# Performance work log

Measured on AMD Instinct MI355X. Metric: run time of the kernel, lower is better.

## Reference

```python
import jax, jax.numpy as jnp
import numpy as np

DIM = 256
HID = 256
EPS = 1e-5

def _layernorm(x, g, b):
    mu = jnp.mean(x, axis=-1, keepdims=True)
    var = jnp.mean(jnp.square(x - mu), axis=-1, keepdims=True)
    return (x - mu) * jax.lax.rsqrt(var + EPS) * g + b

def setup_inputs() -> dict:
    key = jax.random.key(0)
    ks = jax.random.split(key, 6)
    B, N = 2, 512
    x = jax.random.normal(ks[0], (B, N, DIM), dtype=jnp.float32)
    mask = jax.random.randint(ks[1], (B, N), 0, 2).astype(jnp.bool_)
    s_in = 1.0 / np.sqrt(DIM)
    s_h = 1.0 / np.sqrt(HID)
    return {
        "x": x,
        "mask": mask,
        "ln_g": jnp.ones((DIM,), jnp.float32),
        "ln_b": jnp.zeros((DIM,), jnp.float32),
        "Wl": jax.random.uniform(ks[2], (DIM, HID), jnp.float32, -s_in, s_in),
        "bl": jnp.zeros((HID,), jnp.float32),
        "Wo": jax.random.uniform(ks[3], (HID, HID), jnp.float32, -s_h, s_h),
        "bo": jnp.zeros((HID,), jnp.float32),
        "lno_g": jnp.ones((HID,), jnp.float32),
        "lno_b": jnp.zeros((HID,), jnp.float32),
    }

def reference(x, mask, ln_g, ln_b, Wl, bl, Wo, bo, lno_g, lno_b):
    # x: [B, N, D], mask: [B, N] bool
    xn = _layernorm(x, ln_g, ln_b)
    left = xn @ Wl + bl                                  # [B, N, H]
    outer = left[:, :, None, :] * left[:, None, :, :]    # [B, N, N, H]
    m2 = (mask[:, :, None] & mask[:, None, :])[..., None]  # [B, N, N, 1]
    outer = jnp.where(m2, outer, 0.0)
    h = _layernorm(jax.nn.gelu(outer, approximate=False), lno_g, lno_b)
    return h @ Wo + bo                                   # [B, N, N, H]
```

## Files before the change

### kernel.cpp

```cpp
#include <hip/hip_runtime.h>
#include <stdint.h>

#define DIM 256
#define HID 256
#define NSEQ 512
#define NB 2
#define EPS 1e-5f

typedef __attribute__((ext_vector_type(4))) float f32x4;
typedef __attribute__((ext_vector_type(4))) short bf16x4;
typedef __attribute__((ext_vector_type(8))) short bf16x8;

#define DIAG_BLOCKS 512
#define BATCH_BLOCKS 2304

__device__ __forceinline__ unsigned short f2bf(float f) {
    unsigned int u = __float_as_uint(f);
    u += 0x7fffu + ((u >> 16) & 1u);
    return (unsigned short)(u >> 16);
}

__device__ __forceinline__ float bfval(float f) {
    return __uint_as_float((unsigned)f2bf(f) << 16);
}

__device__ __forceinline__ float gelu_fast(float x) {
    const float z  = x * 0.7071067811865476f;
    const float az = fabsf(z);
    const float t  = __builtin_amdgcn_rcpf(fmaf(0.3275911f, az, 1.0f));
    float p = fmaf(1.061405429f, t, -1.453152027f);
    p = fmaf(p, t,  1.421413741f);
    p = fmaf(p, t, -0.284496736f);
    p = fmaf(p, t,  0.254829592f);
    p = p * t;
    const float e = __builtin_amdgcn_exp2f(az * az * -1.4426950408889634f);
    float erfv = fmaf(-p, e, 1.0f);
    erfv = copysignf(erfv, z);
    return 0.5f * x * (1.0f + erfv);
}

__device__ __forceinline__ int pairpos(int k) {
    return ((k >> 5) << 5) + (((k >> 2) & 3) << 3) + (((k >> 4) & 1) << 2) + (k & 3);
}

__global__ __launch_bounds__(256) void prep_kernel(
    const float* __restrict__ x, const void* __restrict__ mask,
    const float* __restrict__ ln_g, const float* __restrict__ ln_b,
    const float* __restrict__ Wl, const float* __restrict__ bl,
    const float* __restrict__ Wo, const float* __restrict__ lno_b,
    const float* __restrict__ bo,
    float* __restrict__ lm, unsigned short* __restrict__ woTp,
    int* __restrict__ maskr, float* __restrict__ cst)
{
    const int row = blockIdx.x;
    const int t = threadIdx.x;
    const int lane = t & 63, w = t >> 6;
    __shared__ float xs[DIM];
    __shared__ float red[8];
    __shared__ int bad_s[4];

    {
        const int v = ((const int*)mask)[t];
        unsigned long long bm = __ballot((v & ~1) != 0);
        if (lane == 0) bad_s[w] = (bm != 0ull) ? 1 : 0;
    }

    float v = x[row * DIM + t];
    float s = v, ss = v * v;
    #pragma unroll
    for (int o = 32; o; o >>= 1) { s += __shfl_xor(s, o); ss += __shfl_xor(ss, o); }
    if (lane == 0) { red[w] = s; red[4 + w] = ss; }
    __syncthreads();
    s  = red[0] + red[1] + red[2] + red[3];
    ss = red[4] + red[5] + red[6] + red[7];
    const float mu  = s * (1.0f / DIM);
    const float var = ss * (1.0f / DIM) - mu * mu;
    const float rs  = rsqrtf(var + EPS);
    xs[t] = (v - mu) * rs * ln_g[t] + ln_b[t];
    __syncthreads();

    float acc = bl[t];
    #pragma unroll 4
    for (int k = 0; k < DIM; k += 4) {
        float4 xv = *(const float4*)&xs[k];
        acc = fmaf(xv.x, Wl[(k + 0) * HID + t], acc);
        acc = fmaf(xv.y, Wl[(k + 1) * HID + t], acc);
        acc = fmaf(xv.z, Wl[(k + 2) * HID + t], acc);
        acc = fmaf(xv.w, Wl[(k + 3) * HID + t], acc);
    }
    const int packed = bad_s[0] | bad_s[1] | bad_s[2] | bad_s[3];
    const int mv = packed ? (int)((const unsigned char*)mask)[row]
                          : ((const int*)mask)[row];
    lm[row * HID + t] = mv ? acc : 0.0f;
    if (t == 0) maskr[row] = mv;

    if (row < HID) {
        woTp[row * HID + pairpos(t)] = f2bf(Wo[t * HID + row]);
    }
    if (row == 0) {
        float c = bo[t];
        for (int k = 0; k < HID; ++k)
            c = fmaf(bfval(lno_b[k]), bfval(Wo[k * HID + t]), c);
        cst[t] = c;
    }
}

__global__ __launch_bounds__(256, 5) void outer_kernel(
    const float* __restrict__ lm, const unsigned short* __restrict__ woTp,
    const float* __restrict__ lno_g, const float* __restrict__ lno_b,
    const float* __restrict__ bo, const int* __restrict__ maskr,
    const float* __restrict__ cst, float* __restrict__ out)
{
    int blk = (int)blockIdx.x;
    int b = 0;
    if (blk >= BATCH_BLOCKS) { b = 1; blk -= BATCH_BLOCKS; }
    int i, jt, mirror;
    if (blk < DIAG_BLOCKS) {
        i = blk; jt = i >> 6; mirror = 0;
    } else {
        const int r2 = blk - DIAG_BLOCKS;
        const int p  = r2 >> 6;
        const int il = r2 & 63;
        int bi = 0, start = 0;
        #pragma unroll
        for (int bb = 0; bb < 7; ++bb) {
            const int s = bb * 7 - (bb * (bb - 1)) / 2;
            if (p >= s) { bi = bb; start = s; }
        }
        const int bj = bi + 1 + (p - start);
        i = bi * 64 + il;
        jt = bj;
        mirror = 1;
    }
    const int j0  = jt * 64;
    const int t    = threadIdx.x;
    const int lane = t & 63;
    const int w    = t >> 6;
    const size_t base = (size_t)(b * NSEQ + i) * NSEQ * HID;

    if (maskr[b * NSEQ + i] == 0) {
        const f32x4 c = *(const f32x4*)&cst[lane * 4];
        #pragma unroll 4
        for (int r = 0; r < 16; ++r) {
            const int j = j0 + w * 16 + r;
            *(f32x4*)&out[base + (size_t)j * HID + lane * 4] = c;
            if (mirror)
                *(f32x4*)&out[((size_t)(b * NSEQ + j) * NSEQ + i) * HID + lane * 4] = c;
        }
        return;
    }

    __shared__ __align__(16) unsigned char ybuf[64 * 512];

    const float4 li4 = *(const float4*)&lm[(size_t)(b * NSEQ + i) * HID + lane * 4];
    const float4 g4  = *(const float4*)&lno_g[lane * 4];
    const float4 bb4 = *(const float4*)&lno_b[lane * 4];

    const int wrb = ((lane >> 3) << 6) + ((lane & 3) << 4) + (((lane >> 2) & 1) << 3);

    const uint2 ucst = make_uint2(
        ((unsigned)f2bf(bb4.y) << 16) | (unsigned)f2bf(bb4.x),
        ((unsigned)f2bf(bb4.w) << 16) | (unsigned)f2bf(bb4.z));

    #pragma unroll 4
    for (int r = 0; r < 16; ++r) {
        const int rl = w * 16 + r;
        const int j  = j0 + rl;
        const int off = rl * 512 + (wrb ^ ((rl & 7) << 4));
        if (maskr[b * NSEQ + j] == 0) {
            *(uint2*)&ybuf[off] = ucst;
            continue;
        }
        float4 lj4 = *(const float4*)&lm[(size_t)(b * NSEQ + j) * HID + lane * 4];
        float4 p;
        p.x = gelu_fast(li4.x * lj4.x);
        p.y = gelu_fast(li4.y * lj4.y);
        p.z = gelu_fast(li4.z * lj4.z);
        p.w = gelu_fast(li4.w * lj4.w);
        float s  = p.x + p.y + p.z + p.w;
        float ss = p.x * p.x + p.y * p.y + p.z * p.z + p.w * p.w;
        #pragma unroll
        for (int o = 32; o; o >>= 1) { s += __shfl_xor(s, o); ss += __shfl_xor(ss, o); }
        const float mu  = s * (1.0f / HID);
        const float var = ss * (1.0f / HID) - mu * mu;
        const float rs  = rsqrtf(var + EPS);
        const float y0 = (p.x - mu) * rs * g4.x + bb4.x;
        const float y1 = (p.y - mu) * rs * g4.y + bb4.y;
        const float y2 = (p.z - mu) * rs * g4.z + bb4.z;
        const float y3 = (p.w - mu) * rs * g4.w + bb4.w;
        const unsigned int u0 = ((unsigned)f2bf(y1) << 16) | (unsigned)f2bf(y0);
        const unsigned int u1 = ((unsigned)f2bf(y3) << 16) | (unsigned)f2bf(y2);
        *(uint2*)&ybuf[off] = make_uint2(u0, u1);
    }
    __syncthreads();

    const int n0  = w * 64;
    const int l15 = lane & 15;
    const int q   = lane >> 4;

    #pragma unroll
    for (int half = 0; half < 2; ++half) {
        f32x4 acc[4][2];
        #pragma unroll
        for (int mi = 0; mi < 4; ++mi)
            #pragma unroll
            for (int nh = 0; nh < 2; ++nh)
                acc[mi][nh] = (f32x4){0.f, 0.f, 0.f, 0.f};

#if !__has_builtin(__builtin_amdgcn_mfma_f32_16x16x16bf16_1k)
        #pragma unroll
        for (int mi = 0; mi < 4; ++mi)
            #pragma unroll
            for (int nh = 0; nh < 2; ++nh)
                asm volatile("" : "+v"(acc[mi][nh]));
        asm volatile("s_nop 1");
#endif

        #pragma unroll
        for (int kk2 = 0; kk2 < 8; ++kk2) {
            const int pb = kk2 * 64 + q * 16;
            bf16x8 a8[4], b8[2];
            #pragma unroll
            for (int mi = 0; mi < 4; ++mi) {
                const int rowm = mi * 16 + l15;
                a8[mi] = *(const bf16x8*)&ybuf[rowm * 512 + (pb ^ ((rowm & 7) << 4))];
            }
            #pragma unroll
            for (int nh = 0; nh < 2; ++nh) {
                const int col = n0 + (half * 2 + nh) * 16 + l15;
                b8[nh] = *(const bf16x8*)&woTp[col * HID + kk2 * 32 + q * 8];
            }
            #pragma unroll
            for (int mi = 0; mi < 4; ++mi) {
                const bf16x4 alo = __builtin_shufflevector(a8[mi], a8[mi], 0, 1, 2, 3);
                const bf16x4 ahi = __builtin_shufflevector(a8[mi], a8[mi], 4, 5, 6, 7);
                #pragma unroll
                for (int nh = 0; nh < 2; ++nh) {
                    const bf16x4 blo = __builtin_shufflevector(b8[nh], b8[nh], 0, 1, 2, 3);
                    const bf16x4 bhi = __builtin_shufflevector(b8[nh], b8[nh], 4, 5, 6, 7);
#if __has_builtin(__builtin_amdgcn_mfma_f32_16x16x16bf16_1k)
                    acc[mi][nh] = __builtin_amdgcn_mfma_f32_16x16x16bf16_1k(
                        blo, alo, acc[mi][nh], 0, 0, 0);
                    acc[mi][nh] = __builtin_amdgcn_mfma_f32_16x16x16bf16_1k(
                        bhi, ahi, acc[mi][nh], 0, 0, 0);
#else
                    asm volatile("v_mfma_f32_16x16x16_bf16 %0, %1, %2, %0"
                                 : "+v"(acc[mi][nh]) : "v"(blo), "v"(alo));
                    asm volatile("v_mfma_f32_16x16x16_bf16 %0, %1, %2, %0"
                                 : "+v"(acc[mi][nh]) : "v"(bhi), "v"(ahi));
#endif
                }
            }
        }

#if !__has_builtin(__builtin_amdgcn_mfma_f32_16x16x16bf16_1k)
        asm volatile("s_nop 7");
        asm volatile("s_nop 7");
        #pragma unroll
        for (int mi = 0; mi < 4; ++mi)
            #pragma unroll
            for (int nh = 0; nh < 2; ++nh)
                asm volatile("" : "+v"(acc[mi][nh]));
#endif

        #pragma unroll
        for (int mi = 0; mi < 4; ++mi) {
            const int j = j0 + mi * 16 + l15;
            const size_t prow = base + (size_t)j * HID;
            const size_t mrow = ((size_t)(b * NSEQ + j) * NSEQ + i) * HID;
            #pragma unroll
            for (int nh = 0; nh < 2; ++nh) {
                const int h0 = n0 + (half * 2 + nh) * 16 + q * 4;
                const float4 bo4 = *(const float4*)&bo[h0];
                f32x4 o;
                o[0] = acc[mi][nh][0] + bo4.x;
                o[1] = acc[mi][nh][1] + bo4.y;
                o[2] = acc[mi][nh][2] + bo4.z;
                o[3] = acc[mi][nh][3] + bo4.w;
                *(f32x4*)&out[prow + h0] = o;
                if (mirror)
                    *(f32x4*)&out[mrow + h0] = o;
            }
        }
    }
}

extern "C" void kernel_launch(void* const* d_in, const int* in_sizes, int n_in,
                              void* d_out, int out_size, void* d_ws, size_t ws_size,
                              hipStream_t stream) {
    (void)in_sizes; (void)n_in; (void)out_size; (void)ws_size;
    const float* x     = (const float*)d_in[0];
    const void*  mask  = d_in[1];
    const float* ln_g  = (const float*)d_in[2];
    const float* ln_b  = (const float*)d_in[3];
    const float* Wl    = (const float*)d_in[4];
    const float* bl    = (const float*)d_in[5];
    const float* Wo    = (const float*)d_in[6];
    const float* bo    = (const float*)d_in[7];
    const float* lno_g = (const float*)d_in[8];
    const float* lno_b = (const float*)d_in[9];

    char* ws = (char*)d_ws;
    float*          lm    = (float*)ws;
    unsigned short* woTp  = (unsigned short*)(ws + (size_t)NB * NSEQ * HID * 4);
    int*            maskr = (int*)(ws + (size_t)NB * NSEQ * HID * 4 + HID * HID * 2);
    float*          cst   = (float*)(ws + (size_t)NB * NSEQ * HID * 4 + HID * HID * 2
                                        + NB * NSEQ * 4);

    prep_kernel<<<NB * NSEQ, 256, 0, stream>>>(x, mask, ln_g, ln_b, Wl, bl, Wo,
                                               lno_b, bo, lm, woTp, maskr, cst);
    outer_kernel<<<NB * BATCH_BLOCKS, 256, 0, stream>>>(
        lm, woTp, lno_g, lno_b, bo, maskr, cst, (float*)d_out);
}
```

Before: 155.1 us.

## Drop symmetric mirroring and compute every (i, j-tile) block directly

Replaces the triangular block schedule, which computed only blocks on or above the diagonal and wrote each result to both (i,j) and (j,i), with a flat grid covering all i and all 64-wide j tiles. Each block now writes only its own contiguous rows, so the strided mirror stores go away and block indexing becomes simple bit arithmetic. In exchange, the number of blocks doing MFMA, GELU and LayerNorm work rises from 4608 to 8192, nearly doubling compute, while total bytes written stay the same.

New measurement: 164.3 us. +5.9%, slower.

```diff
diff --git a/kernel.cpp b/kernel.cpp
--- a/kernel.cpp
+++ b/kernel.cpp
@@ -10,9 +10,6 @@
 typedef __attribute__((ext_vector_type(4))) float f32x4;
 typedef __attribute__((ext_vector_type(4))) short bf16x4;
 typedef __attribute__((ext_vector_type(8))) short bf16x8;
-
-#define DIAG_BLOCKS 512
-#define BATCH_BLOCKS 2304
 
 __device__ __forceinline__ unsigned short f2bf(float f) {
     unsigned int u = __float_as_uint(f);
@@ -111,27 +108,10 @@
     const float* __restrict__ bo, const int* __restrict__ maskr,
     const float* __restrict__ cst, float* __restrict__ out)
 {
-    int blk = (int)blockIdx.x;
-    int b = 0;
-    if (blk >= BATCH_BLOCKS) { b = 1; blk -= BATCH_BLOCKS; }
-    int i, jt, mirror;
-    if (blk < DIAG_BLOCKS) {
-        i = blk; jt = i >> 6; mirror = 0;
-    } else {
-        const int r2 = blk - DIAG_BLOCKS;
-        const int p  = r2 >> 6;
-        const int il = r2 & 63;
-        int bi = 0, start = 0;
-        #pragma unroll
-        for (int bb = 0; bb < 7; ++bb) {
-            const int s = bb * 7 - (bb * (bb - 1)) / 2;
-            if (p >= s) { bi = bb; start = s; }
-        }
-        const int bj = bi + 1 + (p - start);
-        i = bi * 64 + il;
-        jt = bj;
-        mirror = 1;
-    }
+    const int blk = (int)blockIdx.x;
+    const int b   = blk >> 12;
+    const int i   = (blk >> 3) & (NSEQ - 1);
+    const int jt  = blk & 7;
     const int j0  = jt * 64;
     const int t    = threadIdx.x;
     const int lane = t & 63;
@@ -144,8 +124,6 @@
         for (int r = 0; r < 16; ++r) {
             const int j = j0 + w * 16 + r;
             *(f32x4*)&out[base + (size_t)j * HID + lane * 4] = c;
-            if (mirror)
-                *(f32x4*)&out[((size_t)(b * NSEQ + j) * NSEQ + i) * HID + lane * 4] = c;
         }
         return;
     }
@@ -267,7 +245,6 @@
         for (int mi = 0; mi < 4; ++mi) {
             const int j = j0 + mi * 16 + l15;
             const size_t prow = base + (size_t)j * HID;
-            const size_t mrow = ((size_t)(b * NSEQ + j) * NSEQ + i) * HID;
             #pragma unroll
             for (int nh = 0; nh < 2; ++nh) {
                 const int h0 = n0 + (half * 2 + nh) * 16 + q * 4;
@@ -278,8 +255,6 @@
                 o[2] = acc[mi][nh][2] + bo4.z;
                 o[3] = acc[mi][nh][3] + bo4.w;
                 *(f32x4*)&out[prow + h0] = o;
-                if (mirror)
-                    *(f32x4*)&out[mrow + h0] = o;
             }
         }
     }
@@ -309,6 +284,6 @@
 
     prep_kernel<<<NB * NSEQ, 256, 0, stream>>>(x, mask, ln_g, ln_b, Wl, bl, Wo,
                                                lno_b, bo, lm, woTp, maskr, cst);
-    outer_kernel<<<NB * BATCH_BLOCKS, 256, 0, stream>>>(
+    outer_kernel<<<NB * NSEQ * (NSEQ / 64), 256, 0, stream>>>(
         lm, woTp, lno_g, lno_b, bo, maskr, cst, (float*)d_out);
 }
```
